# Kernel tuning notes

Hardware: AMD Instinct MI355X
Metric: run time of the kernel (lower is better)

The kernel has to match this reference:

```python
import jax, jax.numpy as jnp
import numpy as np

EPS = 1e-07
ORTH_LAMBDA = 0.1
KAMA = 1.0


def setup_inputs() -> dict:
    key = jax.random.key(0)
    ks = jax.random.split(key, 10)
    b, c, h, w, n = 8, 128, 128, 128, 16
    s = 0.05  # weight init scale
    return {
        "x":     jax.random.normal(ks[0], (b, c, h, w), jnp.float32),
        "Wsa":   jax.random.normal(ks[1], (c, c), jnp.float32) * s,
        "bsa":   jnp.zeros((c,), jnp.float32),
        "Wr":    jax.random.normal(ks[2], (c, c), jnp.float32) * s,
        "br":    jnp.zeros((c,), jnp.float32),
        "kn":    jax.random.normal(ks[3], (n, c), jnp.float32),  # (nClass, in_c, 1, 1) squeezed
        "Wo":    jax.random.normal(ks[4], (c, c), jnp.float32) * s,
        "bo":    jnp.zeros((c,), jnp.float32),
        "alpha": jnp.ones((1, n, 1), jnp.float32) * 0.1,
        "sigma": jnp.ones((1,), jnp.float32) * 0.5,  # torch inits 0; nonzero so out != x
    }


def reference(x, Wsa, bsa, Wr, br, kn, Wo, bo, alpha, sigma):
    b, c, h, w = x.shape
    n = kn.shape[0]
    hw = h * w

    conv1x1 = lambda W, bb: jnp.einsum('oc,bchw->bohw', W, x) + bb[:, None, None]
    xsa = conv1x1(Wsa, bsa)                       # (b,c,h,w)
    xr = conv1x1(Wr, br)                          # (b,c,h,w)
    xo = conv1x1(Wo, bo)                          # (b,c,h,w)
    xn = jnp.einsum('nc,bchw->bnhw', kn, x)       # (b,n,h,w), no bias

    # ---- orthogonality loss over class kernels ----
    sym = kn @ kn.T                               # (n,n)
    nrm = jnp.sqrt(jnp.sum(kn ** 2, axis=-1, keepdims=True))  # (n,1)
    loss = sym / (nrm @ nrm.T + EPS) - jnp.eye(n, dtype=x.dtype)
    orth_loss = ORTH_LAMBDA * jnp.log(jnp.sum(loss ** 2) + 1.0)

    xsa_r = xsa.reshape(b, c, hw)
    xr_r = xr.reshape(b, c, hw)
    xn_r = xn.reshape(b, n, hw)

    # ---- cosine-normalized class-channel relation ----
    relation = jnp.einsum('bnk,bck->bnc', xn_r, xr_r)            # (b,n,c)
    norm_xr = jnp.sqrt(jnp.sum(xr_r ** 2, axis=-1, keepdims=True))  # (b,c,1)
    norm_xn = jnp.sqrt(jnp.sum(xn_r ** 2, axis=-1, keepdims=True))  # (b,n,1)
    relation_norm = relation / (norm_xn @ jnp.swapaxes(norm_xr, 1, 2) + EPS)

    # ---- channel self-attention regularizer ----
    rela = jnp.einsum('bik,bjk->bij', xsa_r, xsa_r)              # (b,c,c)
    factor = rela * (1.0 - jnp.eye(c, dtype=x.dtype))
    regular = jax.nn.softmax(jnp.mean(factor, axis=1, keepdims=True), axis=-1)  # (b,1,c)

    alpha_c = jnp.clip(alpha, 0.0, 1.0)                          # (1,n,1)
    relation_norm = (relation_norm + alpha_c * regular) / KAMA
    att = jax.nn.softmax(relation_norm, axis=1)                  # (b,n,c)

    # ---- fused attention-weighted group norm (no (b,n,c,h,w) materialization)
    # hot_area[b,n,c,h,w] = xo[b,c,h,w] * att[b,n,c]; reductions over (c,h,w)
    s1 = jnp.sum(xo, axis=(2, 3))                                # (b,c) sum_hw xo
    s2 = jnp.sum(xo ** 2, axis=(2, 3))                           # (b,c) sum_hw xo^2
    cnt = jnp.sum(att, axis=2) * hw + EPS                        # (b,n)
    hot_sum = jnp.einsum('bnc,bc->bn', att, s1)                  # (b,n)
    fo_mean = hot_sum / cnt                                      # (b,n)
    sq = jnp.einsum('bnc,bc->bn', att ** 2, s2) - 2.0 * fo_mean * hot_sum \
         + (fo_mean ** 2) * (c * hw)
    fo_std = jnp.sqrt(sq / cnt)                                  # (b,n)

    # out[b,c,h,w] = sum_n (xo - mean)/(std+eps) * att = xo*A - B
    inv = 1.0 / (fo_std + EPS)                                   # (b,n)
    A = jnp.einsum('bnc,bn->bc', att, inv)                       # (b,c)
    B = jnp.einsum('bnc,bn->bc', att, fo_mean * inv)             # (b,c)
    out = x + sigma * (xo * A[:, :, None, None] - B[:, :, None, None])
    return out, orth_loss
```

## Files before the change

### kernel.cpp

```cpp
#include <hip/hip_runtime.h>
#include <hip/hip_bf16.h>

#define B_   8
#define C_   128
#define HW_  16384
#define N_   16
#define EPS_ 1e-7f

typedef unsigned short u16;
typedef __attribute__((ext_vector_type(8))) short s8v;
typedef __attribute__((ext_vector_type(4))) short s4v;
typedef __attribute__((ext_vector_type(4))) float f4v;

__device__ __forceinline__ u16 f2b(float f) {
  union { __hip_bfloat16 b; u16 u; } cv; cv.b = __float2bfloat16(f); return cv.u;
}
__device__ __forceinline__ float b2f(u16 u) {
  union { float f; unsigned int i; } cv; cv.i = ((unsigned int)u) << 16; return cv.f;
}
__device__ __forceinline__ float wredsum(float v) {
#pragma unroll
  for (int o = 32; o > 0; o >>= 1) v += __shfl_xor(v, o, 64);
  return v;
}
__device__ __forceinline__ float wredmax(float v) {
#pragma unroll
  for (int o = 32; o > 0; o >>= 1) v = fmaxf(v, __shfl_xor(v, o, 64));
  return v;
}

#define XS_ 132
__global__ __launch_bounds__(512, 4) void k_gram(
    const float* __restrict__ x, float* __restrict__ pbuf, float* __restrict__ psx,
    const float* __restrict__ Wsa, const float* __restrict__ kn,
    const float* __restrict__ Wo, float* __restrict__ u,
    float* __restrict__ loss_out, u16* __restrict__ wo_bf) {
  __shared__ u16 Xb[C_ * XS_];
  const int tid = threadIdx.x;
  const int b = blockIdx.y;

  if (blockIdx.x == 64) {
    if (b == 0) {
      if (tid < C_) {
        float s = 0.f;
        for (int i = 0; i < C_; ++i) s += Wsa[i * C_ + tid];
        u[tid] = s;
      }
    } else if (b == 1) {
      float* smf = (float*)Xb;
      const int i = tid >> 4, j = tid & 15;
      float s = 0.f;
      if (tid < 256) {
        for (int c = 0; c < C_; ++c) s += kn[i * C_ + c] * kn[j * C_ + c];
        if (i == j) smf[i] = sqrtf(s);
      }
      __syncthreads();
      float l2 = 0.f;
      if (tid < 256) {
        float l = s / (smf[i] * smf[j] + EPS_) - (i == j ? 1.f : 0.f);
        l2 = l * l;
      }
      float wv = wredsum(l2);
      if ((tid & 63) == 0) smf[16 + (tid >> 6)] = wv;
      __syncthreads();
      if (tid == 0) {
        float t = 0.f;
        for (int k = 0; k < 8; ++k) t += smf[16 + k];
        loss_out[0] = 0.1f * logf(t + 1.f);
      }
    } else if (b == 2) {
#pragma unroll
      for (int j = 0; j < 8; ++j) {
        int f = tid + 512 * j;
        float4 v = ((const float4*)Wo)[f];
        s4v s; s[0] = (short)f2b(v.x); s[1] = (short)f2b(v.y);
        s[2] = (short)f2b(v.z); s[3] = (short)f2b(v.w);
        ((s4v*)wo_bf)[f] = s;
      }
    }
    return;
  }

  const int p0 = blockIdx.x * 256;
  const int lane = tid & 63;
  const int w = tid >> 6;
  const int m = lane & 15, q = lane >> 4;
  const int rb = (w & 3) * 32, cb = (w >> 2) * 64;

  f4v acc[2][4];
#pragma unroll
  for (int a = 0; a < 2; ++a)
#pragma unroll
    for (int c2 = 0; c2 < 4; ++c2) acc[a][c2] = (f4v){0.f, 0.f, 0.f, 0.f};

  const float* xb = x + (size_t)b * C_ * HW_;
  const float* ro = xb + (size_t)(tid >> 5) * HW_ + p0 + 4 * (tid & 31);

  float4 v[8];
#pragma unroll
  for (int j = 0; j < 8; ++j) v[j] = *(const float4*)(ro + (size_t)(16 * j) * HW_);

  float rs[8];
#pragma unroll
  for (int t = 0; t < 2; ++t) {
#pragma unroll
    for (int j = 0; j < 8; ++j) {
      int c = (tid >> 5) + 16 * j;
      s4v s; s[0] = (short)f2b(v[j].x); s[1] = (short)f2b(v[j].y);
      s[2] = (short)f2b(v[j].z); s[3] = (short)f2b(v[j].w);
      *(s4v*)(&Xb[c * XS_ + 4 * (tid & 31)]) = s;
      float rsum = v[j].x + v[j].y + v[j].z + v[j].w;
      if (t == 0) rs[j] = rsum; else rs[j] += rsum;
    }
    __syncthreads();
    if (t == 0) {
#pragma unroll
      for (int j = 0; j < 8; ++j) v[j] = *(const float4*)(ro + (size_t)(16 * j) * HW_ + 128);
    }
#pragma unroll
    for (int s = 0; s < 4; ++s) {
      const int k0 = 32 * s;
      s8v Af[2], Bf[4];
#pragma unroll
      for (int a = 0; a < 2; ++a)
        Af[a] = *(const s8v*)(&Xb[(rb + 16 * a + m) * XS_ + k0 + 8 * q]);
#pragma unroll
      for (int c2 = 0; c2 < 4; ++c2)
        Bf[c2] = *(const s8v*)(&Xb[(cb + 16 * c2 + m) * XS_ + k0 + 8 * q]);
#pragma unroll
      for (int a = 0; a < 2; ++a)
#pragma unroll
        for (int c2 = 0; c2 < 4; ++c2)
          acc[a][c2] = __builtin_amdgcn_mfma_f32_16x16x32_bf16(Af[a], Bf[c2], acc[a][c2], 0, 0, 0);
    }
    __syncthreads();
  }

  f4v* pg4 = (f4v*)pbuf + ((size_t)(blockIdx.x * B_ + b) << 12);
#pragma unroll
  for (int a = 0; a < 2; ++a)
#pragma unroll
    for (int c2 = 0; c2 < 4; ++c2)
      pg4[(w * 8 + a * 4 + c2) * 64 + lane] = acc[a][c2];

#pragma unroll
  for (int o = 16; o > 0; o >>= 1)
#pragma unroll
    for (int j = 0; j < 8; ++j) rs[j] += __shfl_xor(rs[j], o, 64);
  if ((tid & 31) == 0) {
#pragma unroll
    for (int j = 0; j < 8; ++j)
      psx[(blockIdx.x * B_ + b) * C_ + (tid >> 5) + 16 * j] = rs[j];
  }
}

__global__ __launch_bounds__(128) void k_greduce(const f4v* __restrict__ pbuf4,
                                                 const float* __restrict__ psx,
                                                 float* __restrict__ G,
                                                 float* __restrict__ sx) {
  const int blk = blockIdx.x;
  if (blk < 256) {
    const int gid = blk * 128 + threadIdx.x;
    const int b = gid >> 12, i4 = gid & 4095;
    f4v s = (f4v){0.f, 0.f, 0.f, 0.f};
#pragma unroll 16
    for (int ch = 0; ch < 64; ++ch)
      s += pbuf4[((size_t)(ch * B_ + b) << 12) + i4];
    const int w = i4 >> 9, j = (i4 >> 6) & 7, lane = i4 & 63;
    const int a = j >> 2, c2 = j & 3, q = lane >> 4, m = lane & 15;
    const int row0 = (w & 3) * 32 + 16 * a + 4 * q;
    const int col = (w >> 2) * 64 + 16 * c2 + m;
    float* Gp = G + b * C_ * C_ + row0 * C_ + col;
    Gp[0] = s.x; Gp[C_] = s.y; Gp[2 * C_] = s.z; Gp[3 * C_] = s.w;
  } else {
    const int tt = (blk - 256) * 128 + threadIdx.x;
    const int b = tt >> 7, c = tt & 127;
    float s = 0.f;
#pragma unroll 16
    for (int ch = 0; ch < 64; ++ch) s += psx[(ch * B_ + b) * C_ + c];
    sx[tt] = s;
  }
}

__global__ __launch_bounds__(64) void k_cols(
    const float* __restrict__ G, const float* __restrict__ sx,
    const float* __restrict__ Wr, const float* __restrict__ Wsa,
    const float* __restrict__ Wo, const float* __restrict__ kn,
    const float* __restrict__ u,
    float* diagR, float* diagSA, float* colsumSA, float* diagO,
    float* prv, float* psav, float* pov, float* rel, float* diagN, float* ksx) {
  const int b = blockIdx.y;
  const int col = blockIdx.x;
  const int lane = threadIdx.x;
  const float* Gb = G + b * C_ * C_;
  const float4* g0 = (const float4*)(Gb + lane * C_);
  const float4* g1 = (const float4*)(Gb + (64 + lane) * C_);
  const float sx0 = sx[b * C_ + lane], sx1 = sx[b * C_ + 64 + lane];

  if (col < C_) {
    const float4* wr = (const float4*)(Wr + col * C_);
    const float4* wa = (const float4*)(Wsa + col * C_);
    const float4* wo = (const float4*)(Wo + col * C_);
    float t0r = 0, t1r = 0, t0a = 0, t1a = 0, t0o = 0, t1o = 0;
    for (int c = 0; c < 32; ++c) {
      float4 a0 = g0[c], a1 = g1[c];
      float4 vr = wr[c], va = wa[c], vo = wo[c];
      t0r += a0.x * vr.x + a0.y * vr.y + a0.z * vr.z + a0.w * vr.w;
      t1r += a1.x * vr.x + a1.y * vr.y + a1.z * vr.z + a1.w * vr.w;
      t0a += a0.x * va.x + a0.y * va.y + a0.z * va.z + a0.w * va.w;
      t1a += a1.x * va.x + a1.y * va.y + a1.z * va.z + a1.w * va.w;
      t0o += a0.x * vo.x + a0.y * vo.y + a0.z * vo.z + a0.w * vo.w;
      t1o += a1.x * vo.x + a1.y * vo.y + a1.z * vo.z + a1.w * vo.w;
    }
    float wr0 = Wr[col * C_ + lane], wr1 = Wr[col * C_ + 64 + lane];
    float wa0 = Wsa[col * C_ + lane], wa1 = Wsa[col * C_ + 64 + lane];
    float wo0 = Wo[col * C_ + lane], wo1 = Wo[col * C_ + 64 + lane];
    float u0 = u[lane], u1 = u[64 + lane];
    float dR = wredsum(wr0 * t0r + wr1 * t1r);
    float pR = wredsum(wr0 * sx0 + wr1 * sx1);
    float dA = wredsum(wa0 * t0a + wa1 * t1a);
    float cA = wredsum(u0 * t0a + u1 * t1a);
    float pA = wredsum(wa0 * sx0 + wa1 * sx1);
    float dO = wredsum(wo0 * t0o + wo1 * t1o);
    float pO = wredsum(wo0 * sx0 + wo1 * sx1);
    float rl[N_];
#pragma unroll
    for (int n = 0; n < N_; ++n)
      rl[n] = wredsum(kn[n * C_ + lane] * t0r + kn[n * C_ + 64 + lane] * t1r);
    if (lane == 0) {
      diagR[b * C_ + col] = dR;  prv[b * C_ + col] = pR;
      diagSA[b * C_ + col] = dA; colsumSA[b * C_ + col] = cA; psav[b * C_ + col] = pA;
      diagO[b * C_ + col] = dO;  pov[b * C_ + col] = pO;
      for (int n = 0; n < N_; ++n) rel[(b * N_ + n) * C_ + col] = rl[n];
    }
  } else {
    const int n = col - C_;
    const float4* wk = (const float4*)(kn + n * C_);
    float t0 = 0, t1 = 0;
    for (int c = 0; c < 32; ++c) {
      float4 a0 = g0[c], a1 = g1[c], vk = wk[c];
      t0 += a0.x * vk.x + a0.y * vk.y + a0.z * vk.z + a0.w * vk.w;
      t1 += a1.x * vk.x + a1.y * vk.y + a1.z * vk.z + a1.w * vk.w;
    }
    float k0v = kn[n * C_ + lane], k1v = kn[n * C_ + 64 + lane];
    float dN = wredsum(k0v * t0 + k1v * t1);
    float kx = wredsum(k0v * sx0 + k1v * sx1);
    if (lane == 0) { diagN[b * N_ + n] = dN; ksx[b * N_ + n] = kx; }
  }
}

__global__ __launch_bounds__(128) void k_asm(
    const float* diagR, const float* diagSA, const float* colsumSA, const float* diagO,
    const float* prv, const float* psav, const float* pov,
    const float* rel, const float* diagN, const float* ksx,
    const float* br, const float* bo, const float* bsa, const float* alpha,
    const float* sigma, float* C1out, float* C0out) {
  const int b = blockIdx.x;
  const int t = threadIdx.x;
  __shared__ float rb2[2];
  __shared__ float att_s[C_][N_ + 1];
  __shared__ float s1_s[C_], s2_s[C_];
  __shared__ float inv_s[N_], fmi_s[N_];
  const float hw = (float)HW_;
  const float bsa_c = bsa[t], br_c = br[t], bo_c = bo[t];
  const float psa_c = psav[b * C_ + t], pr_c = prv[b * C_ + t], po_c = pov[b * C_ + t];

  float bsum, psum, mx, ssum;
  { float wv = wredsum(bsa_c); if ((t & 63) == 0) rb2[t >> 6] = wv; __syncthreads();
    bsum = rb2[0] + rb2[1]; __syncthreads(); }
  { float wv = wredsum(psa_c); if ((t & 63) == 0) rb2[t >> 6] = wv; __syncthreads();
    psum = rb2[0] + rb2[1]; __syncthreads(); }

  const float nxr = sqrtf(fmaxf(diagR[b * C_ + t] + 2.f * br_c * pr_c + hw * br_c * br_c, 0.f));
  s1_s[t] = po_c + hw * bo_c;
  s2_s[t] = diagO[b * C_ + t] + 2.f * bo_c * po_c + hw * bo_c * bo_c;
  const float colsum = colsumSA[b * C_ + t] + bsum * psa_c + bsa_c * (psum + hw * bsum);
  const float diagv = diagSA[b * C_ + t] + 2.f * bsa_c * psa_c + hw * bsa_c * bsa_c;
  const float fm = (colsum - diagv) * (1.f / (float)C_);

  { float wv = wredmax(fm); if ((t & 63) == 0) rb2[t >> 6] = wv; __syncthreads();
    mx = fmaxf(rb2[0], rb2[1]); __syncthreads(); }
  const float ee = expf(fm - mx);
  { float wv = wredsum(ee); if ((t & 63) == 0) rb2[t >> 6] = wv; __syncthreads();
    ssum = rb2[0] + rb2[1]; __syncthreads(); }
  const float reg = ee / ssum;

  float r[N_];
  float rmax = -1e30f;
#pragma unroll
  for (int n = 0; n < N_; ++n) {
    float al = fminf(fmaxf(alpha[n], 0.f), 1.f);
    float nxn = sqrtf(fmaxf(diagN[b * N_ + n], 0.f));
    float rv = (rel[(b * N_ + n) * C_ + t] + br_c * ksx[b * N_ + n]) / (nxn * nxr + EPS_) + al * reg;
    r[n] = rv; rmax = fmaxf(rmax, rv);
  }
  float es = 0.f;
#pragma unroll
  for (int n = 0; n < N_; ++n) { r[n] = expf(r[n] - rmax); es += r[n]; }
  const float ies = 1.f / es;
#pragma unroll
  for (int n = 0; n < N_; ++n) att_s[t][n] = r[n] * ies;
  __syncthreads();

  {
    const int nn = t >> 3, g = t & 7;
    float sa = 0.f, sh = 0.f, sq = 0.f;
#pragma unroll 4
    for (int c = g; c < C_; c += 8) {
      float a = att_s[c][nn];
      sa += a; sh += a * s1_s[c]; sq += a * a * s2_s[c];
    }
#pragma unroll
    for (int o = 4; o > 0; o >>= 1) {
      sa += __shfl_xor(sa, o, 64);
      sh += __shfl_xor(sh, o, 64);
      sq += __shfl_xor(sq, o, 64);
    }
    if (g == 0) {
      float cnt = sa * hw + EPS_;
      float fmean = sh / cnt;
      float sqv = sq - 2.f * fmean * sh + fmean * fmean * ((float)C_ * hw);
      float fstd = sqrtf(fmaxf(sqv, 0.f) / cnt);
      float inv = 1.f / (fstd + EPS_);
      inv_s[nn] = inv; fmi_s[nn] = fmean * inv;
    }
  }
  __syncthreads();

  float Ac = 0.f, Bc = 0.f;
#pragma unroll
  for (int n = 0; n < N_; ++n) { float a = att_s[t][n]; Ac += a * inv_s[n]; Bc += a * fmi_s[n]; }
  const float sg = sigma[0];
  C1out[b * C_ + t] = sg * Ac;
  C0out[b * C_ + t] = sg * (Ac * bo_c - Bc);
}

#define XT_ 132
__global__ __launch_bounds__(512, 4) void k_out(
    const float* __restrict__ x, const u16* __restrict__ wo_bf,
    const float* __restrict__ c1g, const float* __restrict__ c0g,
    float* __restrict__ out) {
  const int b = blockIdx.y;
  __shared__ u16 Xt[64 * XT_];
  __shared__ float c1s[C_], c0s[C_];
  const int tid = threadIdx.x, lane = tid & 63, w = tid >> 6;
  const int n = lane & 15, q = lane >> 4;

  if (tid < C_) { c1s[tid] = c1g[b * C_ + tid]; c0s[tid] = c0g[b * C_ + tid]; }

  s8v af[4];
#pragma unroll
  for (int s = 0; s < 4; ++s)
    af[s] = *(const s8v*)(wo_bf + (16 * w + n) * C_ + 32 * s + 8 * q);

  const float* xb = x + (size_t)b * C_ * HW_;
  float* ob = out + (size_t)b * C_ * HW_;
  const int pq = tid & 15;
  const int c4 = tid >> 4;

  float4 v[4];
  {
    const int p0 = blockIdx.x * 128;
    const float* src = xb + (size_t)(4 * c4) * HW_ + p0 + 4 * pq;
#pragma unroll
    for (int r2 = 0; r2 < 4; ++r2) v[r2] = *(const float4*)(src + (size_t)r2 * HW_);
  }

#pragma unroll 1
  for (int pt = 0; pt < 2; ++pt) {
    const int p0 = blockIdx.x * 128 + pt * 64;
    {
      float4 v0 = v[0], v1 = v[1], v2 = v[2], v3 = v[3];
      s4v s0, s1, s2, s3;
      s0[0] = (short)f2b(v0.x); s0[1] = (short)f2b(v1.x); s0[2] = (short)f2b(v2.x); s0[3] = (short)f2b(v3.x);
      s1[0] = (short)f2b(v0.y); s1[1] = (short)f2b(v1.y); s1[2] = (short)f2b(v2.y); s1[3] = (short)f2b(v3.y);
      s2[0] = (short)f2b(v0.z); s2[1] = (short)f2b(v1.z); s2[2] = (short)f2b(v2.z); s2[3] = (short)f2b(v3.z);
      s3[0] = (short)f2b(v0.w); s3[1] = (short)f2b(v1.w); s3[2] = (short)f2b(v2.w); s3[3] = (short)f2b(v3.w);
      *(s4v*)(&Xt[(4 * pq + 0) * XT_ + 4 * c4]) = s0;
      *(s4v*)(&Xt[(4 * pq + 1) * XT_ + 4 * c4]) = s1;
      *(s4v*)(&Xt[(4 * pq + 2) * XT_ + 4 * c4]) = s2;
      *(s4v*)(&Xt[(4 * pq + 3) * XT_ + 4 * c4]) = s3;
    }
    __syncthreads();
    if (pt < 1) {
      const float* src = xb + (size_t)(4 * c4) * HW_ + p0 + 64 + 4 * pq;
#pragma unroll
      for (int r2 = 0; r2 < 4; ++r2) v[r2] = *(const float4*)(src + (size_t)r2 * HW_);
    }

    f4v acc[4];
#pragma unroll
    for (int p2 = 0; p2 < 4; ++p2) acc[p2] = (f4v){0.f, 0.f, 0.f, 0.f};
#pragma unroll
    for (int s = 0; s < 4; ++s) {
#pragma unroll
      for (int p2 = 0; p2 < 4; ++p2) {
        s8v bfr = *(const s8v*)(&Xt[(16 * p2 + n) * XT_ + 32 * s + 8 * q]);
        acc[p2] = __builtin_amdgcn_mfma_f32_16x16x32_bf16(af[s], bfr, acc[p2], 0, 0, 0);
      }
    }

#pragma unroll
    for (int p2 = 0; p2 < 4; ++p2)
#pragma unroll
      for (int r = 0; r < 4; ++r) {
        int o = 16 * w + 4 * q + r;
        size_t idx = (size_t)o * HW_ + p0 + 16 * p2 + n;
        ob[idx] = xb[idx] + c1s[o] * acc[p2][r] + c0s[o];
      }
    __syncthreads();
  }
}

extern "C" void kernel_launch(void* const* d_in, const int* in_sizes, int n_in,
                              void* d_out, int out_size, void* d_ws, size_t ws_size,
                              hipStream_t stream) {
  (void)in_sizes; (void)n_in; (void)out_size; (void)ws_size;
  const float* x     = (const float*)d_in[0];
  const float* Wsa   = (const float*)d_in[1];
  const float* bsa   = (const float*)d_in[2];
  const float* Wr    = (const float*)d_in[3];
  const float* br    = (const float*)d_in[4];
  const float* kn    = (const float*)d_in[5];
  const float* Wo    = (const float*)d_in[6];
  const float* bo    = (const float*)d_in[7];
  const float* alpha = (const float*)d_in[8];
  const float* sigma = (const float*)d_in[9];
  float* out = (float*)d_out;
  float* ws  = (float*)d_ws;

  float* G        = ws;
  float* sx       = ws + 131072;
  float* diagR    = ws + 132096;
  float* diagSA   = ws + 133120;
  float* colsumSA = ws + 134144;
  float* diagO    = ws + 135168;
  float* prv      = ws + 136192;
  float* psav     = ws + 137216;
  float* pov      = ws + 138240;
  float* rel      = ws + 139264;
  float* diagN    = ws + 155648;
  float* ksx      = ws + 155776;
  float* u        = ws + 155904;
  float* C1w      = ws + 156032;
  float* C0w      = ws + 157056;
  u16*   wo_bf    = (u16*)(ws + 158080);

  float* pbuf = out;
  float* psx  = out + 8388608;

  k_gram<<<dim3(65, 8), 512, 0, stream>>>(x, pbuf, psx, Wsa, kn, Wo, u,
      out + (size_t)B_ * C_ * HW_, wo_bf);
  k_greduce<<<264, 128, 0, stream>>>((const f4v*)pbuf, psx, G, sx);
  k_cols<<<dim3(144, 8), 64, 0, stream>>>(G, sx, Wr, Wsa, Wo, kn, u,
      diagR, diagSA, colsumSA, diagO, prv, psav, pov, rel, diagN, ksx);
  k_asm<<<8, 128, 0, stream>>>(diagR, diagSA, colsumSA, diagO, prv, psav, pov,
      rel, diagN, ksx, br, bo, bsa, alpha, sigma, C1w, C0w);
  k_out<<<dim3(128, 8), 512, 0, stream>>>(x, wo_bf, C1w, C0w, out);
}
```

Measured before the change: 182.7 us.

## Split Gram pass into 128 chunks and store fp16 partials

The Gram kernel now gives each block 128 pixels instead of 256, doubling the grid to 128 chunks per batch and dropping the two-iteration loop. The occupancy hint rises to 8 blocks per CU. Per-chunk partial Gram tiles are written as fp16 instead of fp32, so the partial buffer stays the same size even with twice as many chunks. The reduce kernel now sums 128 fp16 partials. This is meant to raise parallelism and latency hiding in the memory-bound first pass, at the cost of fp16 rounding (and possible overflow) in the partial sums.

```diff
diff --git a/kernel.cpp b/kernel.cpp
--- a/kernel.cpp
+++ b/kernel.cpp
@@ -1,5 +1,6 @@
 #include <hip/hip_runtime.h>
 #include <hip/hip_bf16.h>
+#include <hip/hip_fp16.h>
 
 #define B_   8
 #define C_   128
@@ -15,8 +16,11 @@
 __device__ __forceinline__ u16 f2b(float f) {
   union { __hip_bfloat16 b; u16 u; } cv; cv.b = __float2bfloat16(f); return cv.u;
 }
-__device__ __forceinline__ float b2f(u16 u) {
-  union { float f; unsigned int i; } cv; cv.i = ((unsigned int)u) << 16; return cv.f;
+__device__ __forceinline__ u16 f2h(float f) {
+  union { __half h; u16 u; } cv; cv.h = __float2half(f); return cv.u;
+}
+__device__ __forceinline__ float h2f(u16 u) {
+  union { __half h; u16 u; } cv; cv.u = u; return __half2float(cv.h);
 }
 __device__ __forceinline__ float wredsum(float v) {
 #pragma unroll
@@ -30,8 +34,8 @@
 }
 
 #define XS_ 132
-__global__ __launch_bounds__(512, 4) void k_gram(
-    const float* __restrict__ x, float* __restrict__ pbuf, float* __restrict__ psx,
+__global__ __launch_bounds__(512, 8) void k_gram(
+    const float* __restrict__ x, u16* __restrict__ pbh, float* __restrict__ psx,
     const float* __restrict__ Wsa, const float* __restrict__ kn,
     const float* __restrict__ Wo, float* __restrict__ u,
     float* __restrict__ loss_out, u16* __restrict__ wo_bf) {
@@ -39,7 +43,7 @@
   const int tid = threadIdx.x;
   const int b = blockIdx.y;
 
-  if (blockIdx.x == 64) {
+  if (blockIdx.x == 128) {
     if (b == 0) {
       if (tid < C_) {
         float s = 0.f;
@@ -81,18 +85,12 @@
     return;
   }
 
-  const int p0 = blockIdx.x * 256;
+  const int p0 = blockIdx.x * 128;
   const int lane = tid & 63;
   const int w = tid >> 6;
   const int m = lane & 15, q = lane >> 4;
   const int rb = (w & 3) * 32, cb = (w >> 2) * 64;
 
-  f4v acc[2][4];
-#pragma unroll
-  for (int a = 0; a < 2; ++a)
-#pragma unroll
-    for (int c2 = 0; c2 < 4; ++c2) acc[a][c2] = (f4v){0.f, 0.f, 0.f, 0.f};
-
   const float* xb = x + (size_t)b * C_ * HW_;
   const float* ro = xb + (size_t)(tid >> 5) * HW_ + p0 + 4 * (tid & 31);
 
@@ -102,46 +100,47 @@
 
   float rs[8];
 #pragma unroll
-  for (int t = 0; t < 2; ++t) {
-#pragma unroll
-    for (int j = 0; j < 8; ++j) {
-      int c = (tid >> 5) + 16 * j;
-      s4v s; s[0] = (short)f2b(v[j].x); s[1] = (short)f2b(v[j].y);
-      s[2] = (short)f2b(v[j].z); s[3] = (short)f2b(v[j].w);
-      *(s4v*)(&Xb[c * XS_ + 4 * (tid & 31)]) = s;
-      float rsum = v[j].x + v[j].y + v[j].z + v[j].w;
-      if (t == 0) rs[j] = rsum; else rs[j] += rsum;
-    }
-    __syncthreads();
-    if (t == 0) {
-#pragma unroll
-      for (int j = 0; j < 8; ++j) v[j] = *(const float4*)(ro + (size_t)(16 * j) * HW_ + 128);
-    }
-#pragma unroll
-    for (int s = 0; s < 4; ++s) {
-      const int k0 = 32 * s;
-      s8v Af[2], Bf[4];
-#pragma unroll
-      for (int a = 0; a < 2; ++a)
-        Af[a] = *(const s8v*)(&Xb[(rb + 16 * a + m) * XS_ + k0 + 8 * q]);
+  for (int j = 0; j < 8; ++j) {
+    int c = (tid >> 5) + 16 * j;
+    s4v s; s[0] = (short)f2b(v[j].x); s[1] = (short)f2b(v[j].y);
+    s[2] = (short)f2b(v[j].z); s[3] = (short)f2b(v[j].w);
+    *(s4v*)(&Xb[c * XS_ + 4 * (tid & 31)]) = s;
+    rs[j] = v[j].x + v[j].y + v[j].z + v[j].w;
+  }
+  __syncthreads();
+
+  f4v acc[2][4];
+#pragma unroll
+  for (int a = 0; a < 2; ++a)
+#pragma unroll
+    for (int c2 = 0; c2 < 4; ++c2) acc[a][c2] = (f4v){0.f, 0.f, 0.f, 0.f};
+
+#pragma unroll
+  for (int s = 0; s < 4; ++s) {
+    const int k0 = 32 * s;
+    s8v Af[2], Bf[4];
+#pragma unroll
+    for (int a = 0; a < 2; ++a)
+      Af[a] = *(const s8v*)(&Xb[(rb + 16 * a + m) * XS_ + k0 + 8 * q]);
+#pragma unroll
+    for (int c2 = 0; c2 < 4; ++c2)
+      Bf[c2] = *(const s8v*)(&Xb[(cb + 16 * c2 + m) * XS_ + k0 + 8 * q]);
+#pragma unroll
+    for (int a = 0; a < 2; ++a)
 #pragma unroll
       for (int c2 = 0; c2 < 4; ++c2)
-        Bf[c2] = *(const s8v*)(&Xb[(cb + 16 * c2 + m) * XS_ + k0 + 8 * q]);
-#pragma unroll
-      for (int a = 0; a < 2; ++a)
-#pragma unroll
-        for (int c2 = 0; c2 < 4; ++c2)
-          acc[a][c2] = __builtin_amdgcn_mfma_f32_16x16x32_bf16(Af[a], Bf[c2], acc[a][c2], 0, 0, 0);
-    }
-    __syncthreads();
-  }
-
-  f4v* pg4 = (f4v*)pbuf + ((size_t)(blockIdx.x * B_ + b) << 12);
+        acc[a][c2] = __builtin_amdgcn_mfma_f32_16x16x32_bf16(Af[a], Bf[c2], acc[a][c2], 0, 0, 0);
+  }
+
+  s4v* pg = (s4v*)pbh + ((size_t)(blockIdx.x * B_ + b) << 12);
 #pragma unroll
   for (int a = 0; a < 2; ++a)
 #pragma unroll
-    for (int c2 = 0; c2 < 4; ++c2)
-      pg4[(w * 8 + a * 4 + c2) * 64 + lane] = acc[a][c2];
+    for (int c2 = 0; c2 < 4; ++c2) {
+      s4v h; h[0] = (short)f2h(acc[a][c2][0]); h[1] = (short)f2h(acc[a][c2][1]);
+      h[2] = (short)f2h(acc[a][c2][2]); h[3] = (short)f2h(acc[a][c2][3]);
+      pg[(w * 8 + a * 4 + c2) * 64 + lane] = h;
+    }
 
 #pragma unroll
   for (int o = 16; o > 0; o >>= 1)
@@ -154,7 +153,7 @@
   }
 }
 
-__global__ __launch_bounds__(128) void k_greduce(const f4v* __restrict__ pbuf4,
+__global__ __launch_bounds__(128) void k_greduce(const s4v* __restrict__ pbh,
                                                  const float* __restrict__ psx,
                                                  float* __restrict__ G,
                                                  float* __restrict__ sx) {
@@ -163,9 +162,12 @@
     const int gid = blk * 128 + threadIdx.x;
     const int b = gid >> 12, i4 = gid & 4095;
     f4v s = (f4v){0.f, 0.f, 0.f, 0.f};
-#pragma unroll 16
-    for (int ch = 0; ch < 64; ++ch)
-      s += pbuf4[((size_t)(ch * B_ + b) << 12) + i4];
+#pragma unroll 8
+    for (int ch = 0; ch < 128; ++ch) {
+      s4v p = pbh[((size_t)(ch * B_ + b) << 12) + i4];
+      s.x += h2f((u16)p[0]); s.y += h2f((u16)p[1]);
+      s.z += h2f((u16)p[2]); s.w += h2f((u16)p[3]);
+    }
     const int w = i4 >> 9, j = (i4 >> 6) & 7, lane = i4 & 63;
     const int a = j >> 2, c2 = j & 3, q = lane >> 4, m = lane & 15;
     const int row0 = (w & 3) * 32 + 16 * a + 4 * q;
@@ -176,8 +178,8 @@
     const int tt = (blk - 256) * 128 + threadIdx.x;
     const int b = tt >> 7, c = tt & 127;
     float s = 0.f;
-#pragma unroll 16
-    for (int ch = 0; ch < 64; ++ch) s += psx[(ch * B_ + b) * C_ + c];
+#pragma unroll 8
+    for (int ch = 0; ch < 128; ++ch) s += psx[(ch * B_ + b) * C_ + c];
     sx[tt] = s;
   }
 }
@@ -446,12 +448,12 @@
   float* C0w      = ws + 157056;
   u16*   wo_bf    = (u16*)(ws + 158080);
 
-  float* pbuf = out;
-  float* psx  = out + 8388608;
-
-  k_gram<<<dim3(65, 8), 512, 0, stream>>>(x, pbuf, psx, Wsa, kn, Wo, u,
+  u16*   pbh = (u16*)out;
+  float* psx = out + 8388608;
+
+  k_gram<<<dim3(129, 8), 512, 0, stream>>>(x, pbh, psx, Wsa, kn, Wo, u,
       out + (size_t)B_ * C_ * HW_, wo_bf);
-  k_greduce<<<264, 128, 0, stream>>>((const f4v*)pbuf, psx, G, sx);
+  k_greduce<<<264, 128, 0, stream>>>((const s4v*)pbh, psx, G, sx);
   k_cols<<<dim3(144, 8), 64, 0, stream>>>(G, sx, Wr, Wsa, Wo, kn, u,
       diagR, diagSA, colsumSA, diagO, prv, psav, pov, rel, diagN, ksx);
   k_asm<<<8, 128, 0, stream>>>(diagR, diagSA, colsumSA, diagO, prv, psav, pov,
```

Measured after the change: 205.1 us. +12.3%, slower.
